# Performance work log

Hardware: AMD Instinct MI355X
Metric: run time of the kernel (lower is better)

Reference implementation:

```python
import jax, jax.numpy as jnp
import numpy as np

DIM = 1536   # model dim
H = 12       # heads
HD = 128     # head dim
S = 3072     # tokens
BLK = 128    # tokens per attention block (window partition size)
NB = S // BLK  # 24 blocks
BH, BW = 6, 4  # spatial block grid (BH*BW == NB, one frame)
WIN = 6      # local window in blocks
TOPK = 128   # top-k block pairs kept per (head, frame)
EPS = 1e-5
SCALE = 1.0 / np.sqrt(HD)


def rmsnorm(x, g):
    return x * jax.lax.rsqrt(jnp.mean(x * x, axis=-1, keepdims=True) + EPS) * g


def rope(x, cos, sin):
    # x: [B,S,DIM]; cos/sin: [S,1,HD//2] -> complex rotation on (real,imag) pairs
    b, s, _ = x.shape
    x = x.reshape(b, s, H, HD // 2, 2)
    xr, xi = x[..., 0], x[..., 1]
    c, sn = cos[None], sin[None]            # [1,S,1,HD//2]
    yr = xr * c - xi * sn
    yi = xr * sn + xi * c
    return jnp.stack([yr, yi], axis=-1).reshape(b, s, H * HD)


def local_block_mask(bh, bw, win):
    # build_local_block_mask_shifted_vec_normal_slide (static, numpy)
    r, c = np.arange(bh), np.arange(bw)
    YY, XX = np.meshgrid(r, c, indexing='ij')
    ra, ca = YY.reshape(-1), XX.reshape(-1)
    hh, hw = win // 2, win // 2
    sr, sc = ra - hh, ca - hw
    er, ec = sr + win - 1, sc + win - 1
    in_r = (ra[None, :] >= sr[:, None]) & (ra[None, :] <= er[:, None])
    in_c = (ca[None, :] >= sc[:, None]) & (ca[None, :] <= ec[:, None])
    return jnp.asarray(in_r & in_c)  # [NB,NB] bool


LOCAL = local_block_mask(BH, BW, WIN)


def draft_block_mask(q, k):
    # generate_draft_block_mask: pooled-QK softmax + per-(head,frame) top-k threshold
    qw = q[0].reshape(NB, BLK, DIM).mean(axis=1)   # [NB,DIM] avgpool over window
    kw = k[0].reshape(NB, BLK, DIM).mean(axis=1)
    qh = qw.reshape(NB, H, HD).transpose(1, 0, 2)  # [H,NB,HD]
    kh = kw.reshape(NB, H, HD).transpose(1, 0, 2)
    scores = jnp.einsum('hld,hmd->hlm', qh, kh) * SCALE  # [H,NB,NB]
    rl, rn = NB // LOCAL.shape[0], NB // LOCAL.shape[1]
    lm = jnp.tile(LOCAL, (rl, rn))                       # [NB,NB]
    scores = jnp.where(lm[None], scores, -jnp.inf)
    attn = jax.nn.softmax(scores, axis=-1)               # rows include self -> finite
    it = 1  # one frame: NB == BH*BW
    flat = attn.reshape(H * it, -1)                      # [H, NB*NB]
    k_top = min(flat.shape[1] - 1, TOPK)
    thr = jax.lax.top_k(flat, k_top + 1)[0][:, -1:]      # (topk+1)-th value
    return (flat > thr).reshape(H, NB, NB)               # bool block mask


def forward(x, wq, bq, wk, bk, wv, bv, wo, bo, gq, gk, freqs_cos, freqs_sin):
    q = rope(rmsnorm(x @ wq.T + bq, gq), freqs_cos, freqs_sin)
    k = rope(rmsnorm(x @ wk.T + bk, gk), freqs_cos, freqs_sin)
    v = x @ wv.T + bv

    bm = jax.lax.stop_gradient(draft_block_mask(q, k))   # [H,NB,NB] (no-grad in torch)
    tok = jnp.repeat(jnp.repeat(bm, BLK, axis=1), BLK, axis=2)  # [H,S,S] token mask

    qh = q.reshape(1, S, H, HD).transpose(0, 2, 1, 3)
    kh = k.reshape(1, S, H, HD).transpose(0, 2, 1, 3)
    vh = v.reshape(1, S, H, HD).transpose(0, 2, 1, 3)

    s = jnp.einsum('bhsd,bhtd->bhst', qh, kh) * SCALE
    s = jnp.where(tok[None], s, -jnp.inf)
    m = jnp.max(s, axis=-1, keepdims=True)
    m = jnp.where(jnp.isfinite(m), m, 0.0)               # guard fully-masked rows
    p = jnp.exp(s - m) * tok[None].astype(s.dtype)
    den = jnp.sum(p, axis=-1, keepdims=True)
    o = jnp.einsum('bhst,bhtd->bhsd', p, vh) / jnp.where(den > 0, den, 1.0)
    o = o.transpose(0, 2, 1, 3).reshape(1, S, DIM)
    return o @ wo.T + bo


def setup_inputs() -> dict:
    key = jax.random.key(0)
    ks = jax.random.split(key, 8)
    w = lambda kk: (jax.random.normal(kk, (DIM, DIM), jnp.float32) * 0.02)
    pos = jnp.arange(S, dtype=jnp.float32)
    inv = 1.0 / (10000.0 ** (jnp.arange(HD // 2, dtype=jnp.float32) / (HD // 2)))
    ang = pos[:, None] * inv[None, :]                    # [S,HD//2]
    return {
        'x': jax.random.normal(ks[0], (1, S, DIM), jnp.float32),
        'wq': w(ks[1]), 'bq': jnp.zeros((DIM,), jnp.float32),
        'wk': w(ks[2]), 'bk': jnp.zeros((DIM,), jnp.float32),
        'wv': w(ks[3]), 'bv': jnp.zeros((DIM,), jnp.float32),
        'wo': w(ks[4]), 'bo': jnp.zeros((DIM,), jnp.float32),
        'gq': jnp.ones((DIM,), jnp.float32),
        'gk': jnp.ones((DIM,), jnp.float32),
        'freqs_cos': jnp.cos(ang)[:, None, :],
        'freqs_sin': jnp.sin(ang)[:, None, :],
    }


def reference(x, wq, bq, wk, bk, wv, bv, wo, bo, gq, gk, freqs_cos, freqs_sin):
    return forward(x, wq, bq, wk, bk, wv, bv, wo, bo, gq, gk, freqs_cos, freqs_sin)
```

## Files before the change

### kernel.cpp

```cpp
#include <hip/hip_runtime.h>
#include <hip/hip_bf16.h>
#include <math.h>

#define SEQ 3072
#define DIM 1536
#define NH 12
#define HD 128
#define NB 24
#define BLKT 128
#define NBSQ 576
#define TOPK_N 128
#define EPSV 1e-5f
#define SCALEV 0.08838834764831845f

typedef __attribute__((ext_vector_type(8))) short short8;
typedef __attribute__((ext_vector_type(4))) short short4v;
typedef __attribute__((ext_vector_type(4))) float f32x4;

typedef __attribute__((address_space(1))) void* gas1_t;
typedef __attribute__((address_space(3))) void* las3_t;

__device__ __forceinline__ float b2f(short u) {
  return __uint_as_float(((unsigned int)(unsigned short)u) << 16);
}
__device__ __forceinline__ short f2b(float x) {
  __hip_bfloat16 h = __float2bfloat16(x);
  return *reinterpret_cast<short*>(&h);
}
__device__ __forceinline__ float ldin(const void* p, size_t i, int f32) {
  return f32 ? ((const float*)p)[i] : b2f(((const short*)p)[i]);
}
__device__ __forceinline__ void gload_lds16(const void* g, void* l) {
  __builtin_amdgcn_global_load_lds((gas1_t)g, (las3_t)l, 16, 0, 0);
}

__global__ __launch_bounds__(256)
void dtype_probe(const void* __restrict__ w, int* __restrict__ flag) {
  __shared__ int cnt;
  if (threadIdx.x == 0) cnt = 0;
  __syncthreads();
  const short* p = (const short*)w;
  int local = 0;
  for (int i = threadIdx.x; i < 4096; i += 256) {
    float v = b2f(p[i]);
    if (!(fabsf(v) <= 1e3f)) local++;
  }
  atomicAdd(&cnt, local);
  __syncthreads();
  if (threadIdx.x == 0) { flag[0] = (cnt > 16) ? 1 : 0; flag[1] = 0; }
}

__device__ __forceinline__ short8 ldchunk(const void* __restrict__ p, size_t idx, int f32) {
  if (f32) {
    const float* q = (const float*)p + idx;
    f32x4 a = *(const f32x4*)q;
    f32x4 b = *(const f32x4*)(q + 4);
    short8 r;
    r[0] = f2b(a[0]); r[1] = f2b(a[1]); r[2] = f2b(a[2]); r[3] = f2b(a[3]);
    r[4] = f2b(b[0]); r[5] = f2b(b[1]); r[6] = f2b(b[2]); r[7] = f2b(b[3]);
    return r;
  }
  return *(const short8*)((const short*)p + idx);
}

__global__ __launch_bounds__(256)
void cvt_bf16(const void* __restrict__ in, short* __restrict__ out, int n8,
              const int* __restrict__ f) {
  int i = blockIdx.x * 256 + threadIdx.x;
  if (i >= n8) return;
  *(short8*)(out + (size_t)i * 8) = ldchunk(in, (size_t)i * 8, *f);
}

#define BK 64

__global__ __launch_bounds__(256)
void gemm128(const short* __restrict__ A,
             const void* __restrict__ W0, const void* __restrict__ W1, const void* __restrict__ W2,
             const void* __restrict__ b0, const void* __restrict__ b1, const void* __restrict__ b2,
             void* __restrict__ C0, void* __restrict__ C1, void* __restrict__ C2,
             int useWB, const int* __restrict__ wfp, const int* __restrict__ ofp) {
  const int fW = *wfp, fO = *ofp;
  __shared__ __attribute__((aligned(16))) short As[128 * BK];
  __shared__ __attribute__((aligned(16))) short Bs[128 * BK];
  const int tid = threadIdx.x;
  const int w = tid >> 6, lane = tid & 63;
  const int lo = lane & 15, hi = lane >> 4;
  const int wr = w >> 1, wc = w & 1;
  const int bx = blockIdx.x;
  const int wsel = bx / 12;
  const int col0 = (bx - wsel * 12) * 128;
  const int row0 = blockIdx.y * 128;
  const void* W = (wsel == 0) ? W0 : ((wsel == 1) ? W1 : W2);
  const void* bb = (wsel == 0) ? b0 : ((wsel == 1) ? b1 : b2);
  void* C = (wsel == 0) ? C0 : ((wsel == 1) ? C1 : C2);

  const f32x4 zero = {0.f, 0.f, 0.f, 0.f};
  f32x4 acc[4][4];
#pragma unroll
  for (int i = 0; i < 4; i++)
#pragma unroll
    for (int j = 0; j < 4; j++) acc[i][j] = zero;

  for (int k0 = 0; k0 < DIM; k0 += BK) {
#pragma unroll
    for (int i = 0; i < 4; i++) {
      int id = i * 256 + tid;
      int r = id >> 3, c = id & 7;
      gload_lds16(A + (size_t)(row0 + r) * DIM + k0 + (c ^ (r & 7)) * 8, &As[id * 8]);
    }
    if (useWB) {
#pragma unroll
      for (int i = 0; i < 4; i++) {
        int id = i * 256 + tid;
        int r = id >> 3, c = id & 7;
        gload_lds16((const short*)W + (size_t)(col0 + r) * DIM + k0 + (c ^ (r & 7)) * 8,
                    &Bs[id * 8]);
      }
    } else {
#pragma unroll
      for (int i = 0; i < 4; i++) {
        int id = i * 256 + tid;
        int r = id >> 3, c = id & 7;
        short8 v = ldchunk(W, (size_t)(col0 + r) * DIM + k0 + c * 8, fW);
        *(short8*)&Bs[r * BK + 8 * (c ^ (r & 7))] = v;
      }
    }
    __syncthreads();
#pragma unroll
    for (int kk = 0; kk < 2; kk++) {
      short8 av[4], bv[4];
#pragma unroll
      for (int mi = 0; mi < 4; mi++) {
        int r = wr * 64 + mi * 16 + lo;
        av[mi] = *(const short8*)&As[r * BK + 8 * ((kk * 4 + hi) ^ (r & 7))];
      }
#pragma unroll
      for (int ni = 0; ni < 4; ni++) {
        int r = wc * 64 + ni * 16 + lo;
        bv[ni] = *(const short8*)&Bs[r * BK + 8 * ((kk * 4 + hi) ^ (r & 7))];
      }
#pragma unroll
      for (int mi = 0; mi < 4; mi++)
#pragma unroll
        for (int ni = 0; ni < 4; ni++)
          acc[mi][ni] = __builtin_amdgcn_mfma_f32_16x16x32_bf16(av[mi], bv[ni], acc[mi][ni], 0, 0, 0);
    }
    __syncthreads();
  }

#pragma unroll
  for (int ni = 0; ni < 4; ni++) {
    int col = col0 + wc * 64 + ni * 16 + lo;
    float bias = ldin(bb, col, fW);
#pragma unroll
    for (int mi = 0; mi < 4; mi++) {
      int rowb = row0 + wr * 64 + mi * 16 + hi * 4;
#pragma unroll
      for (int g = 0; g < 4; g++) {
        float v = acc[mi][ni][g] + bias;
        size_t oi = (size_t)(rowb + g) * DIM + col;
        if (fO) ((float*)C)[oi] = v;
        else    ((short*)C)[oi] = f2b(v);
      }
    }
  }
}

__global__ __launch_bounds__(256)
void rmsnorm_rope_kernel(short* __restrict__ x, const void* __restrict__ g,
                         const void* __restrict__ cs, const void* __restrict__ sn,
                         const int* __restrict__ f) {
  const int fI = *f;
  const int s = blockIdx.x, tid = threadIdx.x;
  short* row = x + (size_t)s * DIM;
  short8 rv = {};
  float ss = 0.f;
  if (tid < 192) {
    rv = *(const short8*)(row + tid * 8);
#pragma unroll
    for (int j = 0; j < 8; j++) { float v = b2f(rv[j]); ss += v * v; }
  }
#pragma unroll
  for (int m = 32; m; m >>= 1) ss += __shfl_xor(ss, m, 64);
  __shared__ float wsum[4];
  if ((tid & 63) == 0) wsum[tid >> 6] = ss;
  __syncthreads();
  float rn = rsqrtf((wsum[0] + wsum[1] + wsum[2] + wsum[3]) * (1.0f / DIM) + EPSV);
  if (tid >= 192) return;
  short8 out;
#pragma unroll
  for (int j = 0; j < 4; j++) {
    int p = tid * 4 + j, pi = p & 63;
    float c  = ldin(cs, (size_t)s * 64 + pi, fI);
    float si = ldin(sn, (size_t)s * 64 + pi, fI);
    float xr = b2f(rv[2 * j])     * rn * ldin(g, tid * 8 + 2 * j, fI);
    float xi = b2f(rv[2 * j + 1]) * rn * ldin(g, tid * 8 + 2 * j + 1, fI);
    out[2 * j]     = f2b(xr * c - xi * si);
    out[2 * j + 1] = f2b(xr * si + xi * c);
  }
  *(short8*)(row + tid * 8) = out;
}

__global__ __launch_bounds__(256)
void pool_kernel(const short* __restrict__ x, float* __restrict__ out) {
  const int nb = blockIdx.x;
  const int d = blockIdx.y * 256 + threadIdx.x;
  float s = 0.f;
  for (int t = 0; t < BLKT; t++) s += b2f(x[(size_t)(nb * BLKT + t) * DIM + d]);
  out[nb * DIM + d] = s * (1.0f / BLKT);
}

__global__ __launch_bounds__(256)
void draft_mask_kernel(const float* __restrict__ qw, const float* __restrict__ kw,
                       int* __restrict__ bm, int* __restrict__ cost) {
  const int h = blockIdx.x, tid = threadIdx.x;
  __shared__ float qh[NB][HD];
  __shared__ float kh[NB][HD];
  __shared__ float attn[NBSQ];
  __shared__ int cw[4];

  for (int idx = tid; idx < NB * HD; idx += 256) {
    int l = idx >> 7, d = idx & 127;
    qh[l][d] = qw[l * DIM + h * HD + d];
    kh[l][d] = kw[l * DIM + h * HD + d];
  }
  __syncthreads();

  for (int idx = tid; idx < NBSQ; idx += 256) {
    int l = idx / NB, m = idx % NB;
    int rl = l >> 2, cl = l & 3, rm = m >> 2, cm = m & 3;
    bool loc = (rm >= rl - 3) && (rm <= rl + 2) && (cm >= cl - 3) && (cm <= cl + 2);
    float sc;
    if (loc) {
      sc = 0.f;
      for (int d = 0; d < HD; d++) sc += qh[l][d] * kh[m][d];
      sc *= SCALEV;
    } else {
      sc = -INFINITY;
    }
    attn[idx] = sc;
  }
  __syncthreads();

  if (tid < NB) {
    float mx = -INFINITY;
    for (int m = 0; m < NB; m++) mx = fmaxf(mx, attn[tid * NB + m]);
    float sm = 0.f;
    for (int m = 0; m < NB; m++) {
      float p = expf(attn[tid * NB + m] - mx);
      attn[tid * NB + m] = p;
      sm += p;
    }
    float inv = 1.0f / sm;
    for (int m = 0; m < NB; m++) attn[tid * NB + m] *= inv;
  }
  __syncthreads();

  unsigned int blo = 0u, bhi = 0x3F800000u;
  while (blo < bhi) {
    unsigned int mid = (blo + bhi) >> 1;
    float t = __uint_as_float(mid);
    int c = 0;
    for (int idx = tid; idx < NBSQ; idx += 256) c += (attn[idx] > t) ? 1 : 0;
#pragma unroll
    for (int m = 1; m < 64; m <<= 1) c += __shfl_xor(c, m, 64);
    if ((tid & 63) == 0) cw[tid >> 6] = c;
    __syncthreads();
    int tot = cw[0] + cw[1] + cw[2] + cw[3];
    if (tot <= TOPK_N) bhi = mid; else blo = mid + 1;
    __syncthreads();
  }
  float thr = __uint_as_float(blo);

  for (int idx = tid; idx < NBSQ; idx += 256)
    bm[h * NBSQ + idx] = (attn[idx] > thr) ? 1 : 0;

  if (tid < NB) {
    int cnt = 0;
    for (int m = 0; m < NB; m++) cnt += (attn[tid * NB + m] > thr) ? 1 : 0;
    cost[h * NB + tid] = cnt;
  }
}

__global__ __launch_bounds__(256)
void order_tasks(const int* __restrict__ cost, int* __restrict__ taskmap) {
  int t = blockIdx.x * 256 + threadIdx.x;
  if (t >= 576) return;
  int xcd = t / 72, base = xcd * 72;
  int h = t / 48, rem = t - h * 48, l = rem >> 1;
  int c = cost[h * NB + l];
  int rank = 0;
  for (int j = 0; j < 72; j++) {
    int tj = base + j;
    int hj = tj / 48, remj = tj - hj * 48, lj = remj >> 1;
    int cj = cost[hj * NB + lj];
    if (cj > c || (cj == c && tj < t)) rank++;
  }
  taskmap[base + rank] = t;
}

__global__ __launch_bounds__(256)
void transpose_kernel(const short* __restrict__ v, short* __restrict__ vt) {
  __shared__ short tile[64][68];
  const int s0 = blockIdx.x * 64, c0 = blockIdx.y * 64;
  const int tid = threadIdx.x;
#pragma unroll
  for (int i = 0; i < 4; i++) {
    int id = i * 256 + tid;
    int r = id >> 4, cq = (id & 15) * 4;
    *(short4v*)&tile[r][cq] = *(const short4v*)(v + (size_t)(s0 + r) * DIM + c0 + cq);
  }
  __syncthreads();
#pragma unroll
  for (int i = 0; i < 4; i++) {
    int id = i * 256 + tid;
    int d = id >> 4, sq = (id & 15) * 4;
    short4v val;
#pragma unroll
    for (int jj = 0; jj < 4; jj++) val[jj] = tile[sq + jj][d];
    *(short4v*)(vt + (size_t)(c0 + d) * SEQ + s0 + sq) = val;
  }
}

__global__ __launch_bounds__(256)
void attn_mfma(const short* __restrict__ q, const short* __restrict__ k,
               const short* __restrict__ vt, const int* __restrict__ bm,
               short* __restrict__ o, int* __restrict__ ctr,
               const int* __restrict__ taskmap) {
  const int xcd = blockIdx.x & 7;
  const int tid = threadIdx.x;
  const int w = tid >> 6;
  const int lane = tid & 63;
  const int lo = lane & 15, hi = lane >> 4;

  __shared__ __attribute__((aligned(16))) short Ks[128 * 128];
  __shared__ __attribute__((aligned(16))) short Vs[128 * 128];
  __shared__ __attribute__((aligned(16))) short Ps[4][16 * 128];
  __shared__ int tsh;

  const f32x4 zero = {0.f, 0.f, 0.f, 0.f};
  const int sr = tid >> 4, sc = tid & 15;

  for (;;) {
    if (tid == 0) tsh = atomicAdd(&ctr[xcd * 8], 1);
    __syncthreads();
    const int slot = tsh;
    if (slot >= 72) break;
    const int t = taskmap[xcd * 72 + slot];
    const int h = t / 48;
    const int rem = t - h * 48;
    const int l = rem >> 1, half = rem & 1;

    const int* bmrow = bm + h * NBSQ + l * NB;
    const short* kh = k + h * HD;
    const short* vth = vt + (size_t)h * HD * SEQ;

    const int qt = l * 8 + half * 4 + w;
    const int qrow = qt * 16 + lo;
    short8 qa[4];
#pragma unroll
    for (int kk = 0; kk < 4; kk++)
      qa[kk] = *(const short8*)(q + (size_t)qrow * DIM + h * HD + kk * 32 + hi * 8);

    f32x4 oacc[8];
#pragma unroll
    for (int i = 0; i < 8; i++) oacc[i] = zero;
    float m_i[4] = {-INFINITY, -INFINITY, -INFINITY, -INFINITY};
    float l_i[4] = {0.f, 0.f, 0.f, 0.f};

    short8 kreg[8], vreg[8];
    int jc = 0;
    while (jc < NB && !bmrow[jc]) jc++;
    if (jc < NB) {
      const int t0 = jc * BLKT;
#pragma unroll
      for (int i = 0; i < 8; i++) {
        int r = i * 16 + sr;
        kreg[i] = *(const short8*)(kh + (size_t)(t0 + r) * DIM + sc * 8);
        vreg[i] = *(const short8*)(vth + (size_t)r * SEQ + t0 + sc * 8);
      }
    }

    while (jc < NB) {
#pragma unroll
      for (int i = 0; i < 8; i++) {
        int r = i * 16 + sr;
        *(short8*)&Ks[r * 128 + 8 * (sc ^ (r & 7))] = kreg[i];
        *(short8*)&Vs[r * 128 + 8 * (sc ^ (r & 7))] = vreg[i];
      }
      __syncthreads();

      int jn = jc + 1;
      while (jn < NB && !bmrow[jn]) jn++;
      if (jn < NB) {
        const int t0 = jn * BLKT;
#pragma unroll
        for (int i = 0; i < 8; i++) {
          int r = i * 16 + sr;
          kreg[i] = *(const short8*)(kh + (size_t)(t0 + r) * DIM + sc * 8);
          vreg[i] = *(const short8*)(vth + (size_t)r * SEQ + t0 + sc * 8);
        }
      }

      f32x4 S[8];
#pragma unroll
      for (int tt = 0; tt < 8; tt++) {
        f32x4 s = zero;
#pragma unroll
        for (int kk = 0; kk < 4; kk++) {
          int rt = tt * 16 + lo;
          short8 kb = *(const short8*)&Ks[rt * 128 + 8 * ((kk * 4 + hi) ^ (rt & 7))];
          s = __builtin_amdgcn_mfma_f32_16x16x32_bf16(qa[kk], kb, s, 0, 0, 0);
        }
        S[tt] = s;
      }

      float alpha[4];
#pragma unroll
      for (int g = 0; g < 4; g++) {
        float mx = S[0][g];
#pragma unroll
        for (int tt = 1; tt < 8; tt++) mx = fmaxf(mx, S[tt][g]);
#pragma unroll
        for (int msk = 1; msk < 16; msk <<= 1) mx = fmaxf(mx, __shfl_xor(mx, msk, 16));
        mx *= SCALEV;
        float mn = fmaxf(m_i[g], mx);
        alpha[g] = __expf(m_i[g] - mn);
        float ps = 0.f;
        int r = hi * 4 + g;
#pragma unroll
        for (int tt = 0; tt < 8; tt++) {
          float p = __expf(S[tt][g] * SCALEV - mn);
          ps += p;
          int t2 = tt * 16 + lo;
          Ps[w][r * 128 + 8 * ((t2 >> 3) ^ (r & 7)) + (t2 & 7)] = f2b(p);
        }
#pragma unroll
        for (int msk = 1; msk < 16; msk <<= 1) ps += __shfl_xor(ps, msk, 16);
        l_i[g] = l_i[g] * alpha[g] + ps;
        m_i[g] = mn;
      }
#pragma unroll
      for (int dt = 0; dt < 8; dt++) {
        f32x4 tv = oacc[dt];
        tv[0] *= alpha[0]; tv[1] *= alpha[1]; tv[2] *= alpha[2]; tv[3] *= alpha[3];
        oacc[dt] = tv;
      }

#pragma unroll
      for (int kk = 0; kk < 4; kk++) {
        int ch = kk * 4 + hi;
        short8 pa = *(const short8*)&Ps[w][lo * 128 + 8 * (ch ^ (lo & 7))];
#pragma unroll
        for (int dt = 0; dt < 8; dt++) {
          int rd = dt * 16 + lo;
          short8 vb = *(const short8*)&Vs[rd * 128 + 8 * (ch ^ (rd & 7))];
          oacc[dt] = __builtin_amdgcn_mfma_f32_16x16x32_bf16(pa, vb, oacc[dt], 0, 0, 0);
        }
      }
      __syncthreads();
      jc = jn;
    }

    float inv[4];
#pragma unroll
    for (int g = 0; g < 4; g++) inv[g] = (l_i[g] > 0.f) ? 1.f / l_i[g] : 0.f;
#pragma unroll
    for (int dt = 0; dt < 8; dt++)
#pragma unroll
      for (int g = 0; g < 4; g++)
        o[(size_t)(qt * 16 + hi * 4 + g) * DIM + h * HD + dt * 16 + lo] =
            f2b(oacc[dt][g] * inv[g]);
    __syncthreads();
  }
}

extern "C" void kernel_launch(void* const* d_in, const int* in_sizes, int n_in,
                              void* d_out, int out_size, void* d_ws, size_t ws_size,
                              hipStream_t stream) {
  char* wsb = (char*)d_ws;
  int*   flag = (int*)(wsb + 0);
  int*   ctr  = (int*)(wsb + 64);
  int*   cost = (int*)(wsb + 384);
  int*   tmap = (int*)(wsb + 1536);
  float* qw   = (float*)(wsb + 4096);
  float* kw   = (float*)(wsb + 4096 + 147456);
  int*   bm   = (int*)(wsb + 4096 + 294912);
  const size_t base = 327680;
  short* q16 = (short*)(wsb + base);
  short* k16 = q16 + (size_t)SEQ * DIM;
  short* v16 = k16 + (size_t)SEQ * DIM;
  short* xb  = v16 + (size_t)SEQ * DIM;
  short* vt  = xb;
  short* o16 = v16;

  const int bigws = (ws_size >= (size_t)56 * 1024 * 1024) ? 1 : 0;
  short* wqb = xb + (size_t)SEQ * DIM;
  short* wkb = wqb + (size_t)DIM * DIM;
  short* wvb = wkb + (size_t)DIM * DIM;
  short* wob = wqb;

  dtype_probe<<<1, 256, 0, stream>>>(d_in[1], flag);
  hipMemsetAsync(ctr, 0, 256, stream);

  const int n8x = SEQ * DIM / 8;
  const int n8w = DIM * DIM / 8;
  cvt_bf16<<<n8x / 256, 256, 0, stream>>>(d_in[0], xb, n8x, flag);
  if (bigws) {
    cvt_bf16<<<n8w / 256, 256, 0, stream>>>(d_in[1], wqb, n8w, flag);
    cvt_bf16<<<n8w / 256, 256, 0, stream>>>(d_in[3], wkb, n8w, flag);
    cvt_bf16<<<n8w / 256, 256, 0, stream>>>(d_in[5], wvb, n8w, flag);
  }

  gemm128<<<dim3(36, SEQ / 128), 256, 0, stream>>>(
      xb,
      bigws ? (const void*)wqb : d_in[1],
      bigws ? (const void*)wkb : d_in[3],
      bigws ? (const void*)wvb : d_in[5],
      d_in[2], d_in[4], d_in[6],
      q16, k16, v16,
      bigws, flag, flag + 1);

  rmsnorm_rope_kernel<<<SEQ, 256, 0, stream>>>(q16, d_in[9],  d_in[11], d_in[12], flag);
  rmsnorm_rope_kernel<<<SEQ, 256, 0, stream>>>(k16, d_in[10], d_in[11], d_in[12], flag);

  pool_kernel<<<dim3(NB, DIM / 256), 256, 0, stream>>>(q16, qw);
  pool_kernel<<<dim3(NB, DIM / 256), 256, 0, stream>>>(k16, kw);

  draft_mask_kernel<<<NH, 256, 0, stream>>>(qw, kw, bm, cost);
  order_tasks<<<3, 256, 0, stream>>>(cost, tmap);

  transpose_kernel<<<dim3(SEQ / 64, DIM / 64), 256, 0, stream>>>(v16, vt);
  if (bigws) cvt_bf16<<<n8w / 256, 256, 0, stream>>>(d_in[7], wob, n8w, flag);

  attn_mfma<<<512, 256, 0, stream>>>(q16, k16, vt, bm, o16, ctr, tmap);

  gemm128<<<dim3(12, SEQ / 128), 256, 0, stream>>>(
      o16,
      bigws ? (const void*)wob : d_in[7], bigws ? (const void*)wob : d_in[7],
      bigws ? (const void*)wob : d_in[7],
      d_in[8], d_in[8], d_in[8],
      d_out, d_out, d_out,
      bigws, flag, flag);
}
```

Baseline: 376.1 us.

## Fuse V transpose into QKV GEMM epilogue and merge paired launches

The QKV GEMM now writes V directly in transposed layout, which removes the separate transpose kernel. The three weight conversions, the two rmsnorm/rope launches and the two pool launches are each merged into one multi-grid launch. The draft-mask top-k threshold changes from a bitwise binary search with many barriers to a rank count over the 576 scores. Attention reuses the P shared buffer to hold the task slot, and workspace buffers are reassigned. The transposed epilogue writes 4-element strided stores, which may coalesce less well.

```diff
diff --git a/kernel.cpp b/kernel.cpp
--- a/kernel.cpp
+++ b/kernel.cpp
@@ -71,6 +71,18 @@
   *(short8*)(out + (size_t)i * 8) = ldchunk(in, (size_t)i * 8, *f);
 }
 
+__global__ __launch_bounds__(256)
+void cvt_bf16_w(const void* __restrict__ i0, const void* __restrict__ i1,
+                const void* __restrict__ i2, short* __restrict__ o0,
+                short* __restrict__ o1, short* __restrict__ o2, int n8,
+                const int* __restrict__ f) {
+  const void* in = (blockIdx.y == 0) ? i0 : ((blockIdx.y == 1) ? i1 : i2);
+  short* out = (blockIdx.y == 0) ? o0 : ((blockIdx.y == 1) ? o1 : o2);
+  int i = blockIdx.x * 256 + threadIdx.x;
+  if (i >= n8) return;
+  *(short8*)(out + (size_t)i * 8) = ldchunk(in, (size_t)i * 8, *f);
+}
+
 #define BK 64
 
 __global__ __launch_bounds__(256)
@@ -78,7 +90,8 @@
              const void* __restrict__ W0, const void* __restrict__ W1, const void* __restrict__ W2,
              const void* __restrict__ b0, const void* __restrict__ b1, const void* __restrict__ b2,
              void* __restrict__ C0, void* __restrict__ C1, void* __restrict__ C2,
-             int useWB, const int* __restrict__ wfp, const int* __restrict__ ofp) {
+             int useWB, const int* __restrict__ wfp, const int* __restrict__ ofp,
+             int vtr) {
   const int fW = *wfp, fO = *ofp;
   __shared__ __attribute__((aligned(16))) short As[128 * BK];
   __shared__ __attribute__((aligned(16))) short Bs[128 * BK];
@@ -148,6 +161,24 @@
     __syncthreads();
   }
 
+  if (vtr && wsel == 2) {
+    short* vtC = (short*)C;
+#pragma unroll
+    for (int ni = 0; ni < 4; ni++) {
+      int col = col0 + wc * 64 + ni * 16 + lo;
+      float bias = ldin(bb, col, fW);
+#pragma unroll
+      for (int mi = 0; mi < 4; mi++) {
+        int rowb = row0 + wr * 64 + mi * 16 + hi * 4;
+        short4v pk;
+#pragma unroll
+        for (int g = 0; g < 4; g++) pk[g] = f2b(acc[mi][ni][g] + bias);
+        *(short4v*)(vtC + (size_t)col * SEQ + rowb) = pk;
+      }
+    }
+    return;
+  }
+
 #pragma unroll
   for (int ni = 0; ni < 4; ni++) {
     int col = col0 + wc * 64 + ni * 16 + lo;
@@ -167,10 +198,13 @@
 }
 
 __global__ __launch_bounds__(256)
-void rmsnorm_rope_kernel(short* __restrict__ x, const void* __restrict__ g,
-                         const void* __restrict__ cs, const void* __restrict__ sn,
-                         const int* __restrict__ f) {
+void rmsnorm_rope2(short* __restrict__ qx, short* __restrict__ kx,
+                   const void* __restrict__ gq, const void* __restrict__ gk,
+                   const void* __restrict__ cs, const void* __restrict__ sn,
+                   const int* __restrict__ f) {
   const int fI = *f;
+  short* x = blockIdx.y ? kx : qx;
+  const void* g = blockIdx.y ? gk : gq;
   const int s = blockIdx.x, tid = threadIdx.x;
   short* row = x + (size_t)s * DIM;
   short8 rv = {};
@@ -202,7 +236,10 @@
 }
 
 __global__ __launch_bounds__(256)
-void pool_kernel(const short* __restrict__ x, float* __restrict__ out) {
+void pool2(const short* __restrict__ qx, const short* __restrict__ kx,
+           float* __restrict__ qw, float* __restrict__ kw) {
+  const short* x = blockIdx.z ? kx : qx;
+  float* out = blockIdx.z ? kw : qw;
   const int nb = blockIdx.x;
   const int d = blockIdx.y * 256 + threadIdx.x;
   float s = 0.f;
@@ -217,7 +254,7 @@
   __shared__ float qh[NB][HD];
   __shared__ float kh[NB][HD];
   __shared__ float attn[NBSQ];
-  __shared__ int cw[4];
+  __shared__ float mw[4];
 
   for (int idx = tid; idx < NB * HD; idx += 256) {
     int l = idx >> 7, d = idx & 127;
@@ -256,21 +293,18 @@
   }
   __syncthreads();
 
-  unsigned int blo = 0u, bhi = 0x3F800000u;
-  while (blo < bhi) {
-    unsigned int mid = (blo + bhi) >> 1;
-    float t = __uint_as_float(mid);
-    int c = 0;
-    for (int idx = tid; idx < NBSQ; idx += 256) c += (attn[idx] > t) ? 1 : 0;
-#pragma unroll
-    for (int m = 1; m < 64; m <<= 1) c += __shfl_xor(c, m, 64);
-    if ((tid & 63) == 0) cw[tid >> 6] = c;
-    __syncthreads();
-    int tot = cw[0] + cw[1] + cw[2] + cw[3];
-    if (tot <= TOPK_N) bhi = mid; else blo = mid + 1;
-    __syncthreads();
-  }
-  float thr = __uint_as_float(blo);
+  float best = INFINITY;
+  for (int base = tid; base < NBSQ; base += 256) {
+    float v = attn[base];
+    int cnt = 0;
+    for (int j = 0; j < NBSQ; j++) cnt += (attn[j] > v) ? 1 : 0;
+    if (cnt <= TOPK_N) best = fminf(best, v);
+  }
+#pragma unroll
+  for (int m = 1; m < 64; m <<= 1) best = fminf(best, __shfl_xor(best, m, 64));
+  if ((tid & 63) == 0) mw[tid >> 6] = best;
+  __syncthreads();
+  float thr = fminf(fminf(mw[0], mw[1]), fminf(mw[2], mw[3]));
 
   for (int idx = tid; idx < NBSQ; idx += 256)
     bm[h * NBSQ + idx] = (attn[idx] > thr) ? 1 : 0;
@@ -300,29 +334,6 @@
 }
 
 __global__ __launch_bounds__(256)
-void transpose_kernel(const short* __restrict__ v, short* __restrict__ vt) {
-  __shared__ short tile[64][68];
-  const int s0 = blockIdx.x * 64, c0 = blockIdx.y * 64;
-  const int tid = threadIdx.x;
-#pragma unroll
-  for (int i = 0; i < 4; i++) {
-    int id = i * 256 + tid;
-    int r = id >> 4, cq = (id & 15) * 4;
-    *(short4v*)&tile[r][cq] = *(const short4v*)(v + (size_t)(s0 + r) * DIM + c0 + cq);
-  }
-  __syncthreads();
-#pragma unroll
-  for (int i = 0; i < 4; i++) {
-    int id = i * 256 + tid;
-    int d = id >> 4, sq = (id & 15) * 4;
-    short4v val;
-#pragma unroll
-    for (int jj = 0; jj < 4; jj++) val[jj] = tile[sq + jj][d];
-    *(short4v*)(vt + (size_t)(c0 + d) * SEQ + s0 + sq) = val;
-  }
-}
-
-__global__ __launch_bounds__(256)
 void attn_mfma(const short* __restrict__ q, const short* __restrict__ k,
                const short* __restrict__ vt, const int* __restrict__ bm,
                short* __restrict__ o, int* __restrict__ ctr,
@@ -335,16 +346,18 @@
 
   __shared__ __attribute__((aligned(16))) short Ks[128 * 128];
   __shared__ __attribute__((aligned(16))) short Vs[128 * 128];
-  __shared__ __attribute__((aligned(16))) short Ps[4][16 * 128];
-  __shared__ int tsh;
+  __shared__ __attribute__((aligned(16))) short Ps[4][2048];
+
+  int* tshp = (int*)&Ps[0][0];
+  short* Pw = Ps[w];
 
   const f32x4 zero = {0.f, 0.f, 0.f, 0.f};
   const int sr = tid >> 4, sc = tid & 15;
 
   for (;;) {
-    if (tid == 0) tsh = atomicAdd(&ctr[xcd * 8], 1);
+    if (tid == 0) *tshp = atomicAdd(&ctr[xcd * 8], 1);
     __syncthreads();
-    const int slot = tsh;
+    const int slot = *tshp;
     if (slot >= 72) break;
     const int t = taskmap[xcd * 72 + slot];
     const int h = t / 48;
@@ -433,7 +446,7 @@
           float p = __expf(S[tt][g] * SCALEV - mn);
           ps += p;
           int t2 = tt * 16 + lo;
-          Ps[w][r * 128 + 8 * ((t2 >> 3) ^ (r & 7)) + (t2 & 7)] = f2b(p);
+          Pw[r * 128 + 8 * ((t2 >> 3) ^ (r & 7)) + (t2 & 7)] = f2b(p);
         }
 #pragma unroll
         for (int msk = 1; msk < 16; msk <<= 1) ps += __shfl_xor(ps, msk, 16);
@@ -450,7 +463,7 @@
 #pragma unroll
       for (int kk = 0; kk < 4; kk++) {
         int ch = kk * 4 + hi;
-        short8 pa = *(const short8*)&Ps[w][lo * 128 + 8 * (ch ^ (lo & 7))];
+        short8 pa = *(const short8*)&Pw[lo * 128 + 8 * (ch ^ (lo & 7))];
 #pragma unroll
         for (int dt = 0; dt < 8; dt++) {
           int rd = dt * 16 + lo;
@@ -489,10 +502,9 @@
   const size_t base = 327680;
   short* q16 = (short*)(wsb + base);
   short* k16 = q16 + (size_t)SEQ * DIM;
-  short* v16 = k16 + (size_t)SEQ * DIM;
-  short* xb  = v16 + (size_t)SEQ * DIM;
-  short* vt  = xb;
-  short* o16 = v16;
+  short* vt  = k16 + (size_t)SEQ * DIM;
+  short* xb  = vt + (size_t)SEQ * DIM;
+  short* o16 = xb;
 
   const int bigws = (ws_size >= (size_t)56 * 1024 * 1024) ? 1 : 0;
   short* wqb = xb + (size_t)SEQ * DIM;
@@ -507,9 +519,8 @@
   const int n8w = DIM * DIM / 8;
   cvt_bf16<<<n8x / 256, 256, 0, stream>>>(d_in[0], xb, n8x, flag);
   if (bigws) {
-    cvt_bf16<<<n8w / 256, 256, 0, stream>>>(d_in[1], wqb, n8w, flag);
-    cvt_bf16<<<n8w / 256, 256, 0, stream>>>(d_in[3], wkb, n8w, flag);
-    cvt_bf16<<<n8w / 256, 256, 0, stream>>>(d_in[5], wvb, n8w, flag);
+    cvt_bf16_w<<<dim3(n8w / 256, 3), 256, 0, stream>>>(
+        d_in[1], d_in[3], d_in[5], wqb, wkb, wvb, n8w, flag);
   }
 
   gemm128<<<dim3(36, SEQ / 128), 256, 0, stream>>>(
@@ -518,19 +529,17 @@
       bigws ? (const void*)wkb : d_in[3],
       bigws ? (const void*)wvb : d_in[5],
       d_in[2], d_in[4], d_in[6],
-      q16, k16, v16,
-      bigws, flag, flag + 1);
-
-  rmsnorm_rope_kernel<<<SEQ, 256, 0, stream>>>(q16, d_in[9],  d_in[11], d_in[12], flag);
-  rmsnorm_rope_kernel<<<SEQ, 256, 0, stream>>>(k16, d_in[10], d_in[11], d_in[12], flag);
-
-  pool_kernel<<<dim3(NB, DIM / 256), 256, 0, stream>>>(q16, qw);
-  pool_kernel<<<dim3(NB, DIM / 256), 256, 0, stream>>>(k16, kw);
+      q16, k16, vt,
+      bigws, flag, flag + 1, 1);
+
+  rmsnorm_rope2<<<dim3(SEQ, 2), 256, 0, stream>>>(q16, k16, d_in[9], d_in[10],
+                                                  d_in[11], d_in[12], flag);
+
+  pool2<<<dim3(NB, DIM / 256, 2), 256, 0, stream>>>(q16, k16, qw, kw);
 
   draft_mask_kernel<<<NH, 256, 0, stream>>>(qw, kw, bm, cost);
   order_tasks<<<3, 256, 0, stream>>>(cost, tmap);
 
-  transpose_kernel<<<dim3(SEQ / 64, DIM / 64), 256, 0, stream>>>(v16, vt);
   if (bigws) cvt_bf16<<<n8w / 256, 256, 0, stream>>>(d_in[7], wob, n8w, flag);
 
   attn_mfma<<<512, 256, 0, stream>>>(q16, k16, vt, bm, o16, ctr, tmap);
@@ -541,5 +550,5 @@
       bigws ? (const void*)wob : d_in[7],
       d_in[8], d_in[8], d_in[8],
       d_out, d_out, d_out,
-      bigws, flag, flag);
-}
+      bigws, flag, flag, 0);
+}
```

Result: faster. 354.3 us (-5.8%).
